# Kernel tuning notes

Measured on AMD Instinct MI355X. Metric: run time of the kernel, lower is better.

The kernel has to match this reference:

```python
import jax, jax.numpy as jnp
import numpy as np

HIDDEN = 1024
HEADS = 16
HEAD_DIM = HIDDEN // HEADS


def setup_inputs() -> dict:
    key = jax.random.key(0)
    ks = jax.random.split(key, 4)
    B, S, H = 2, 2048, HIDDEN
    scale = 1.0 / np.sqrt(H)
    return {
        "inputs": jax.random.normal(ks[0], (B, S, H), dtype=jnp.float32),
        "mask": jnp.ones((B, S), dtype=jnp.int32),
        "Wq": jax.random.normal(ks[1], (H, H), dtype=jnp.float32) * scale,
        "bq": jnp.zeros((H,), dtype=jnp.float32),
        "Wk": jax.random.normal(ks[2], (H, H), dtype=jnp.float32) * scale,
        "bk": jnp.zeros((H,), dtype=jnp.float32),
        "Wv": jax.random.normal(ks[3], (H, H), dtype=jnp.float32) * scale,
        "bv": jnp.zeros((H,), dtype=jnp.float32),
    }


def _split_heads(x, B, S):
    # [B,S,H] -> [B,heads,S,head_dim]
    return x.reshape(B, S, HEADS, HEAD_DIM).transpose(0, 2, 1, 3)


def reference(inputs, mask, Wq, bq, Wk, bk, Wv, bv):
    B, S, H = inputs.shape
    q = _split_heads(inputs @ Wq.T + bq, B, S)
    k = _split_heads(inputs @ Wk.T + bk, B, S)
    v = _split_heads(inputs @ Wv.T + bv, B, S)
    scores = jnp.einsum("bhqd,bhkd->bhqk", q, k) / jnp.sqrt(
        jnp.asarray(HEAD_DIM, dtype=inputs.dtype))
    # mask broadcast [B,1,1,S]; zeros -> -inf
    scores = jnp.where(mask[:, None, None, :] == 0, -jnp.inf, scores)
    attn = jax.nn.softmax(scores, axis=-1)
    context = jnp.einsum("bhqk,bhkd->bhqd", attn, v)
    return context.transpose(0, 2, 1, 3).reshape(B, S, H)
```

## Files before the change

kernel.cpp:

```cpp
#include <hip/hip_runtime.h>
#include <hip/hip_fp16.h>

constexpr int S_LEN  = 2048;
constexpr int HID    = 1024;
constexpr int HEADS  = 16;
constexpr int HDIM   = 64;
constexpr int BATCH  = 2;
constexpr int BH     = BATCH * HEADS;
constexpr int M_ROWS = BATCH * S_LEN;

typedef _Float16 half8  __attribute__((ext_vector_type(8)));
typedef _Float16 half4v __attribute__((ext_vector_type(4)));
typedef _Float16 half2v __attribute__((ext_vector_type(2)));
typedef float    f32x4  __attribute__((ext_vector_type(4)));
typedef float    f32x16 __attribute__((ext_vector_type(16)));
typedef unsigned uint4v __attribute__((ext_vector_type(4)));

constexpr float EXP2_OFF = -11.541560327111707f;
constexpr float Q_SCALE  = 0.18033688011112042f;

__global__ __launch_bounds__(256) void cvt_kernel(
    const float* __restrict__ X,  const float* __restrict__ Wq,
    const float* __restrict__ Wk, const float* __restrict__ Wv,
    const int* __restrict__ mask,
    _Float16* __restrict__ Xh,  _Float16* __restrict__ Wqh,
    _Float16* __restrict__ Wkh, _Float16* __restrict__ Wvh,
    float* __restrict__ maskF)
{
    const int blk = blockIdx.x;
    if (blk >= 3584) {
        const int loc = blk - 3584;
        const size_t e = ((size_t)loc * 256 + threadIdx.x) * 8;
        #pragma unroll
        for (int i = 0; i < 8; ++i)
            maskF[e + i] = mask[e + i] ? EXP2_OFF : -1.0e30f;
        return;
    }
    const float* src; _Float16* dst; int loc;
    if (blk < 2048)      { src = X;  dst = Xh;  loc = blk; }
    else if (blk < 2560) { src = Wq; dst = Wqh; loc = blk - 2048; }
    else if (blk < 3072) { src = Wk; dst = Wkh; loc = blk - 2560; }
    else                 { src = Wv; dst = Wvh; loc = blk - 3072; }
    const size_t e = ((size_t)loc * 256 + threadIdx.x) * 8;
    float4 a = *reinterpret_cast<const float4*>(&src[e]);
    float4 b = *reinterpret_cast<const float4*>(&src[e + 4]);
    half8 h = { (_Float16)a.x, (_Float16)a.y, (_Float16)a.z, (_Float16)a.w,
                (_Float16)b.x, (_Float16)b.y, (_Float16)b.z, (_Float16)b.w };
    *reinterpret_cast<half8*>(&dst[e]) = h;
}

__device__ __forceinline__ void async_cp16(_Float16* lds, const _Float16* g) {
    __builtin_amdgcn_global_load_lds(
        (const __attribute__((address_space(1))) void*)g,
        (__attribute__((address_space(3))) void*)lds, 16, 0, 0);
}
__device__ __forceinline__ void async_cp4(float* lds, const float* g) {
    __builtin_amdgcn_global_load_lds(
        (const __attribute__((address_space(1))) void*)g,
        (__attribute__((address_space(3))) void*)lds, 4, 0, 0);
}

__device__ __forceinline__ void permlane32_swap(unsigned &x, unsigned &y) {
    asm("v_permlane32_swap_b32 %0, %1" : "+v"(x), "+v"(y));
}

__global__ __launch_bounds__(256) void qkv_proj_kernel(
    const _Float16* __restrict__ Xh,
    const _Float16* __restrict__ Wqh, const _Float16* __restrict__ Wkh,
    const _Float16* __restrict__ Wvh,
    const float* __restrict__ bq, const float* __restrict__ bk,
    const float* __restrict__ bv,
    _Float16* __restrict__ Qo, _Float16* __restrict__ Ko,
    _Float16* __restrict__ Vt)
{
    const int mode = blockIdx.z;
    const _Float16* W    = (mode == 0) ? Wqh : (mode == 1) ? Wkh : Wvh;
    const float*    bias = (mode == 0) ? bq  : (mode == 1) ? bk  : bv;

    const int m0 = blockIdx.x * 128, n0 = blockIdx.y * 128;
    const int tid = threadIdx.x, wave = tid >> 6, lane = tid & 63;
    const int l31 = lane & 31, kg = lane >> 5;

    __shared__ _Float16 SMEM[18432];

    f32x16 acc[2][2];
    #pragma unroll
    for (int mt = 0; mt < 2; ++mt)
        #pragma unroll
        for (int nt = 0; nt < 2; ++nt)
            #pragma unroll
            for (int i = 0; i < 16; ++i) acc[mt][nt][i] = 0.f;

    const int wm = (wave & 1) * 64, wn = (wave >> 1) * 64;

    const int srow = tid >> 2, spos = tid & 3;
    auto stage = [&](int k0, int b) {
        _Float16* Asb = SMEM + b * 8192;
        _Float16* Bsb = Asb + 4096;
        #pragma unroll
        for (int j = 0; j < 2; ++j) {
            const int row = srow + j * 64;
            const int sch = spos ^ (row & 3);
            async_cp16(&Asb[j * 2048 + tid * 8],
                       &Xh[(size_t)(m0 + row) * HID + k0 + sch * 8]);
            async_cp16(&Bsb[j * 2048 + tid * 8],
                       &W [(size_t)(n0 + row) * HID + k0 + sch * 8]);
        }
    };

    stage(0, 0);
    int buf = 0;

    for (int k0 = 0; k0 < HID; k0 += 32) {
        __syncthreads();
        if (k0 + 32 < HID) stage(k0 + 32, buf ^ 1);
        _Float16* Asb = SMEM + buf * 8192;
        _Float16* Bsb = Asb + 4096;

        #pragma unroll
        for (int c = 0; c < 2; ++c) {
            const int k8 = c * 2 + kg;
            half8 af[2], bf[2];
            #pragma unroll
            for (int mt = 0; mt < 2; ++mt) {
                const int row = wm + mt * 32 + l31;
                af[mt] = *reinterpret_cast<const half8*>(
                    &Asb[row * 32 + ((k8 ^ (row & 3)) * 8)]);
            }
            #pragma unroll
            for (int nt = 0; nt < 2; ++nt) {
                const int row = wn + nt * 32 + l31;
                bf[nt] = *reinterpret_cast<const half8*>(
                    &Bsb[row * 32 + ((k8 ^ (row & 3)) * 8)]);
            }
            #pragma unroll
            for (int mt = 0; mt < 2; ++mt)
                #pragma unroll
                for (int nt = 0; nt < 2; ++nt)
                    acc[mt][nt] = __builtin_amdgcn_mfma_f32_32x32x16_f16(
                        af[mt], bf[nt], acc[mt][nt], 0, 0, 0);
        }
        buf ^= 1;
    }
    __syncthreads();

    _Float16* T = SMEM + wave * 4608;

    const int nn  = n0 + wn;
    const int hh  = nn >> 6;
    const int mm  = m0 + wm;
    const int bb  = mm >> 11;
    const int bhv = bb * HEADS + hh;
    const int s0  = mm & 2047;
    const int rowg = lane >> 3, chunk = lane & 7;

    if (mode < 2) {
        _Float16* Out = (mode == 0) ? Qo : Ko;
        #pragma unroll
        for (int nt = 0; nt < 2; ++nt) {
            const int col = nt * 32 + l31;
            float bias_n = bias[nn + col];
            #pragma unroll
            for (int mt = 0; mt < 2; ++mt)
                #pragma unroll
                for (int r = 0; r < 16; ++r) {
                    const int row_l = (r & 3) + 8 * (r >> 2) + 4 * kg;
                    float v = acc[mt][nt][r] + bias_n;
                    if (mode == 0) v *= Q_SCALE;
                    T[(mt * 32 + row_l) * 72 + col] = (_Float16)v;
                }
        }
        asm volatile("s_waitcnt lgkmcnt(0)" ::: "memory");
        #pragma unroll
        for (int j = 0; j < 8; ++j) {
            const int sr = j * 8 + rowg;
            half8 v = *reinterpret_cast<const half8*>(&T[sr * 72 + chunk * 8]);
            *reinterpret_cast<half8*>(
                &Out[((size_t)bhv * S_LEN + s0 + sr) * HDIM + chunk * 8]) = v;
        }
    } else {
        #pragma unroll
        for (int nt = 0; nt < 2; ++nt) {
            const int col = nt * 32 + l31;
            const float bias_n = bias[nn + col];
            #pragma unroll
            for (int mt = 0; mt < 2; ++mt)
                #pragma unroll
                for (int rg = 0; rg < 4; ++rg) {
                    half4v t = { (_Float16)(acc[mt][nt][rg * 4 + 0] + bias_n),
                                 (_Float16)(acc[mt][nt][rg * 4 + 1] + bias_n),
                                 (_Float16)(acc[mt][nt][rg * 4 + 2] + bias_n),
                                 (_Float16)(acc[mt][nt][rg * 4 + 3] + bias_n) };
                    const int s_off = mt * 32 + 8 * rg + 4 * kg;
                    *reinterpret_cast<half4v*>(&T[col * 72 + s_off]) = t;
                }
        }
        asm volatile("s_waitcnt lgkmcnt(0)" ::: "memory");
        #pragma unroll
        for (int j = 0; j < 8; ++j) {
            const int dr = j * 8 + rowg;
            half8 v = *reinterpret_cast<const half8*>(&T[dr * 72 + chunk * 8]);
            *reinterpret_cast<half8*>(
                &Vt[((size_t)bhv * HDIM + dr) * S_LEN + s0 + chunk * 8]) = v;
        }
    }
}

__global__ __launch_bounds__(256) void attn_kernel(
    const _Float16* __restrict__ Q, const _Float16* __restrict__ K,
    const _Float16* __restrict__ Vt, const float* __restrict__ maskF,
    float* __restrict__ Out)
{
    const int id   = blockIdx.x;
    const int xcd  = id & 7;
    const int bh   = xcd * 4 + ((id >> 3) & 3);
    const int qt   = id >> 5;
    const int b = bh >> 4, h = bh & 15;
    const int tid = threadIdx.x, wave = tid >> 6, lane = tid & 63;
    const int l31 = lane & 31, kg = lane >> 5;

    __shared__ _Float16 Ks[3][64 * 64];
    __shared__ _Float16 Vs[3][64 * 64];
    __shared__ float    Ms[3][4][64];

    const _Float16* Qb = Q  + (size_t)bh * S_LEN * HDIM;
    const _Float16* Kb = K  + (size_t)bh * S_LEN * HDIM;
    const _Float16* Vb = Vt + (size_t)bh * HDIM * S_LEN;
    const float*    mb = maskF + b * S_LEN;

    const int qrow = qt * 128 + wave * 32 + l31;

    half8 qf[4];
    #pragma unroll
    for (int kc = 0; kc < 4; ++kc)
        qf[kc] = *reinterpret_cast<const half8*>(
            &Qb[(size_t)qrow * HDIM + kc * 16 + kg * 8]);
    asm volatile("s_waitcnt vmcnt(0)" ::: "memory");

    f32x16 acc[2];
    #pragma unroll
    for (int dt = 0; dt < 2; ++dt)
        #pragma unroll
        for (int i = 0; i < 16; ++i) acc[dt][i] = 0.f;
    float den = 0.f;

    const int srow_t = tid >> 3;
    const int slot   = tid & 7;
    auto stage = [&](int tile, int bufsel) {
        const int kb = tile * 64;
        #pragma unroll
        for (int j = 0; j < 2; ++j) {
            const int row  = srow_t + j * 32;
            const int csrc = slot ^ (row & 7);
            async_cp16(&Ks[bufsel][j * 2048 + tid * 8],
                       &Kb[(size_t)(kb + row) * HDIM + csrc * 8]);
            async_cp16(&Vs[bufsel][j * 2048 + tid * 8],
                       &Vb[(size_t)row * S_LEN + kb + csrc * 8]);
        }
        async_cp4(&Ms[bufsel][wave][lane], &mb[kb + lane]);
    };

    constexpr int NT = S_LEN / 64;
    stage(0, 0);
    stage(1, 1);
    int buf = 0;
    const int rsw = l31 & 7;

    for (int t = 0; t < NT; ++t) {
        asm volatile("s_waitcnt vmcnt(5)" ::: "memory");
        __builtin_amdgcn_s_barrier();
        asm volatile("" ::: "memory");

        {
            int nt2 = t + 2; if (nt2 >= NT) nt2 -= NT;
            int nb  = buf + 2; if (nb >= 3) nb -= 3;
            stage(nt2, nb);
        }

        const _Float16* Kl = Ks[buf];
        const _Float16* Vl = Vs[buf];
        const float*    Mw = Ms[buf][wave];

        f32x16 sc[2];
        #pragma unroll
        for (int kt = 0; kt < 2; ++kt) {
            #pragma unroll
            for (int i = 0; i < 16; ++i) sc[kt][i] = 0.f;
            half8 kf[4];
            #pragma unroll
            for (int kc = 0; kc < 4; ++kc)
                kf[kc] = *reinterpret_cast<const half8*>(
                    &Kl[(kt * 32 + l31) * 64 + (((kc * 2 + kg) ^ rsw) * 8)]);
            __builtin_amdgcn_s_setprio(1);
            #pragma unroll
            for (int kc = 0; kc < 4; ++kc)
                sc[kt] = __builtin_amdgcn_mfma_f32_32x32x16_f16(
                    kf[kc], qf[kc], sc[kt], 0, 0, 0);
            __builtin_amdgcn_s_setprio(0);
        }

        half8 vf[2][4];
        #pragma unroll
        for (int dt = 0; dt < 2; ++dt)
            #pragma unroll
            for (int kc = 0; kc < 4; ++kc)
                vf[dt][kc] = *reinterpret_cast<const half8*>(
                    &Vl[(dt * 32 + l31) * 64 + (((kc * 2 + kg) ^ rsw) * 8)]);

        #pragma unroll
        for (int kt = 0; kt < 2; ++kt) {
            float4 mm[4];
            #pragma unroll
            for (int g = 0; g < 4; ++g)
                mm[g] = *reinterpret_cast<const float4*>(
                    &Mw[kt * 32 + g * 8 + kg * 4]);

            float p[16];
            #pragma unroll
            for (int r = 0; r < 16; ++r) {
                const float* m4 = reinterpret_cast<const float*>(&mm[r >> 2]);
                p[r] = __builtin_amdgcn_exp2f(sc[kt][r] + m4[r & 3]);
            }
            den += (((p[0] + p[1]) + (p[2] + p[3])) +
                    ((p[4] + p[5]) + (p[6] + p[7]))) +
                   (((p[8] + p[9]) + (p[10] + p[11])) +
                    ((p[12] + p[13]) + (p[14] + p[15])));

            #pragma unroll
            for (int hh = 0; hh < 2; ++hh) {
                unsigned a0 = __builtin_bit_cast(unsigned,
                    __builtin_amdgcn_cvt_pkrtz(p[hh * 8 + 0], p[hh * 8 + 1]));
                unsigned a1 = __builtin_bit_cast(unsigned,
                    __builtin_amdgcn_cvt_pkrtz(p[hh * 8 + 2], p[hh * 8 + 3]));
                unsigned b0 = __builtin_bit_cast(unsigned,
                    __builtin_amdgcn_cvt_pkrtz(p[hh * 8 + 4], p[hh * 8 + 5]));
                unsigned b1 = __builtin_bit_cast(unsigned,
                    __builtin_amdgcn_cvt_pkrtz(p[hh * 8 + 6], p[hh * 8 + 7]));
                permlane32_swap(a0, b0);
                permlane32_swap(a1, b1);
                uint4v pd = { a0, a1, b0, b1 };
                half8 pf = __builtin_bit_cast(half8, pd);
                const int kc2 = kt * 2 + hh;
                __builtin_amdgcn_s_setprio(1);
                acc[0] = __builtin_amdgcn_mfma_f32_32x32x16_f16(
                    vf[0][kc2], pf, acc[0], 0, 0, 0);
                acc[1] = __builtin_amdgcn_mfma_f32_32x32x16_f16(
                    vf[1][kc2], pf, acc[1], 0, 0, 0);
                __builtin_amdgcn_s_setprio(0);
            }
        }
        if (++buf == 3) buf = 0;
    }

    den += __shfl_xor(den, 32, 64);
    const float inv = 1.0f / den;

    float* orow = Out + ((size_t)(b * S_LEN + qrow)) * HID + h * HDIM;
    #pragma unroll
    for (int dt = 0; dt < 2; ++dt)
        #pragma unroll
        for (int g = 0; g < 4; ++g) {
            float4 o = { acc[dt][g * 4 + 0] * inv, acc[dt][g * 4 + 1] * inv,
                         acc[dt][g * 4 + 2] * inv, acc[dt][g * 4 + 3] * inv };
            *reinterpret_cast<float4*>(&orow[dt * 32 + g * 8 + kg * 4]) = o;
        }
}

extern "C" void kernel_launch(void* const* d_in, const int* in_sizes, int n_in,
                              void* d_out, int out_size, void* d_ws, size_t ws_size,
                              hipStream_t stream) {
    const float* X  = (const float*)d_in[0];
    const int*   mk = (const int*)  d_in[1];
    const float* Wq = (const float*)d_in[2];
    const float* bq = (const float*)d_in[3];
    const float* Wk = (const float*)d_in[4];
    const float* bk = (const float*)d_in[5];
    const float* Wv = (const float*)d_in[6];
    const float* bv = (const float*)d_in[7];
    float* out = (float*)d_out;

    _Float16* Xh  = (_Float16*)d_ws;
    _Float16* Wqh = Xh  + (size_t)M_ROWS * HID;
    _Float16* Wkh = Wqh + (size_t)HID * HID;
    _Float16* Wvh = Wkh + (size_t)HID * HID;
    _Float16* Q   = Wvh + (size_t)HID * HID;
    _Float16* K   = Q   + (size_t)BH * S_LEN * HDIM;
    _Float16* Vt  = K   + (size_t)BH * S_LEN * HDIM;
    float*    maskF = (float*)(Vt + (size_t)BH * S_LEN * HDIM);

    cvt_kernel<<<3586, 256, 0, stream>>>(X, Wq, Wk, Wv, mk, Xh, Wqh, Wkh, Wvh, maskF);

    dim3 gp(M_ROWS / 128, HID / 128, 3);
    qkv_proj_kernel<<<gp, 256, 0, stream>>>(Xh, Wqh, Wkh, Wvh, bq, bk, bv, Q, K, Vt);

    attn_kernel<<<512, 256, 0, stream>>>(Q, K, Vt, maskF, out);
}
```

Measured before the change: 179.2 us.

## Split attention key tiles across two wave groups with LDS reduction

Attention blocks grow from 4 to 8 waves. Each pair of waves shares a 32-row query strip and takes one half of every 64-key tile, so each wave does half the QK and PV MFMA work per tile. Partial accumulators and denominators are summed through shared memory at the end. The mask is now preloaded into the score accumulator instead of added before exp, saving per-element adds. This adds more waves per CU to hide latency, at the cost of extra barriers, an LDS reduction and higher register-limited occupancy pressure.

```diff
diff --git a/kernel.cpp b/kernel.cpp
--- a/kernel.cpp
+++ b/kernel.cpp
@@ -206,7 +206,7 @@
     }
 }
 
-__global__ __launch_bounds__(256) void attn_kernel(
+__global__ __launch_bounds__(512, 4) void attn_kernel(
     const _Float16* __restrict__ Q, const _Float16* __restrict__ K,
     const _Float16* __restrict__ Vt, const float* __restrict__ maskF,
     float* __restrict__ Out)
@@ -218,17 +218,17 @@
     const int b = bh >> 4, h = bh & 15;
     const int tid = threadIdx.x, wave = tid >> 6, lane = tid & 63;
     const int l31 = lane & 31, kg = lane >> 5;
-
-    __shared__ _Float16 Ks[3][64 * 64];
-    __shared__ _Float16 Vs[3][64 * 64];
-    __shared__ float    Ms[3][4][64];
+    const int wq = wave & 3, wk = wave >> 2;
+
+    __shared__ _Float16 SMEM[3 * 8192];
+    __shared__ float    Ms[3][8][64];
 
     const _Float16* Qb = Q  + (size_t)bh * S_LEN * HDIM;
     const _Float16* Kb = K  + (size_t)bh * S_LEN * HDIM;
     const _Float16* Vb = Vt + (size_t)bh * HDIM * S_LEN;
     const float*    mb = maskF + b * S_LEN;
 
-    const int qrow = qt * 128 + wave * 32 + l31;
+    const int qrow = qt * 128 + wq * 32 + l31;
 
     half8 qf[4];
     #pragma unroll
@@ -244,19 +244,15 @@
         for (int i = 0; i < 16; ++i) acc[dt][i] = 0.f;
     float den = 0.f;
 
-    const int srow_t = tid >> 3;
-    const int slot   = tid & 7;
+    const int srow = tid >> 3;
+    const int slot = tid & 7;
     auto stage = [&](int tile, int bufsel) {
-        const int kb = tile * 64;
-        #pragma unroll
-        for (int j = 0; j < 2; ++j) {
-            const int row  = srow_t + j * 32;
-            const int csrc = slot ^ (row & 7);
-            async_cp16(&Ks[bufsel][j * 2048 + tid * 8],
-                       &Kb[(size_t)(kb + row) * HDIM + csrc * 8]);
-            async_cp16(&Vs[bufsel][j * 2048 + tid * 8],
-                       &Vb[(size_t)row * S_LEN + kb + csrc * 8]);
-        }
+        const int kb   = tile * 64;
+        const int csrc = slot ^ (srow & 7);
+        _Float16* Kd = SMEM + bufsel * 8192;
+        _Float16* Vd = Kd + 4096;
+        async_cp16(&Kd[tid * 8], &Kb[(size_t)(kb + srow) * HDIM + csrc * 8]);
+        async_cp16(&Vd[tid * 8], &Vb[(size_t)srow * S_LEN + kb + csrc * 8]);
         async_cp4(&Ms[bufsel][wave][lane], &mb[kb + lane]);
     };
 
@@ -267,7 +263,7 @@
     const int rsw = l31 & 7;
 
     for (int t = 0; t < NT; ++t) {
-        asm volatile("s_waitcnt vmcnt(5)" ::: "memory");
+        asm volatile("s_waitcnt vmcnt(3)" ::: "memory");
         __builtin_amdgcn_s_barrier();
         asm volatile("" ::: "memory");
 
@@ -277,93 +273,111 @@
             stage(nt2, nb);
         }
 
-        const _Float16* Kl = Ks[buf];
-        const _Float16* Vl = Vs[buf];
+        const _Float16* Kl = SMEM + buf * 8192;
+        const _Float16* Vl = Kl + 4096;
         const float*    Mw = Ms[buf][wave];
 
-        f32x16 sc[2];
-        #pragma unroll
-        for (int kt = 0; kt < 2; ++kt) {
-            #pragma unroll
-            for (int i = 0; i < 16; ++i) sc[kt][i] = 0.f;
-            half8 kf[4];
-            #pragma unroll
-            for (int kc = 0; kc < 4; ++kc)
-                kf[kc] = *reinterpret_cast<const half8*>(
-                    &Kl[(kt * 32 + l31) * 64 + (((kc * 2 + kg) ^ rsw) * 8)]);
+        float4 mm0 = *reinterpret_cast<const float4*>(&Mw[wk * 32 + 0 + kg * 4]);
+        float4 mm1 = *reinterpret_cast<const float4*>(&Mw[wk * 32 + 8 + kg * 4]);
+        float4 mm2 = *reinterpret_cast<const float4*>(&Mw[wk * 32 + 16 + kg * 4]);
+        float4 mm3 = *reinterpret_cast<const float4*>(&Mw[wk * 32 + 24 + kg * 4]);
+        f32x16 sc = { mm0.x, mm0.y, mm0.z, mm0.w,
+                      mm1.x, mm1.y, mm1.z, mm1.w,
+                      mm2.x, mm2.y, mm2.z, mm2.w,
+                      mm3.x, mm3.y, mm3.z, mm3.w };
+
+        const _Float16* Krow = &Kl[(wk * 32 + l31) * 64];
+        half8 kf[4];
+        #pragma unroll
+        for (int kc = 0; kc < 4; ++kc)
+            kf[kc] = *reinterpret_cast<const half8*>(
+                &Krow[((kc * 2 + kg) ^ rsw) * 8]);
+        __builtin_amdgcn_s_setprio(1);
+        #pragma unroll
+        for (int kc = 0; kc < 4; ++kc)
+            sc = __builtin_amdgcn_mfma_f32_32x32x16_f16(kf[kc], qf[kc], sc, 0, 0, 0);
+        __builtin_amdgcn_s_setprio(0);
+
+        half8 vf[2][2];
+        #pragma unroll
+        for (int dt = 0; dt < 2; ++dt) {
+            const _Float16* Vrow = &Vl[(dt * 32 + l31) * 64];
+            #pragma unroll
+            for (int hh = 0; hh < 2; ++hh)
+                vf[dt][hh] = *reinterpret_cast<const half8*>(
+                    &Vrow[((wk * 4 + hh * 2 + kg) ^ rsw) * 8]);
+        }
+
+        float p[16];
+        #pragma unroll
+        for (int r = 0; r < 16; ++r)
+            p[r] = __builtin_amdgcn_exp2f(sc[r]);
+        den += (((p[0] + p[1]) + (p[2] + p[3])) +
+                ((p[4] + p[5]) + (p[6] + p[7]))) +
+               (((p[8] + p[9]) + (p[10] + p[11])) +
+                ((p[12] + p[13]) + (p[14] + p[15])));
+
+        #pragma unroll
+        for (int hh = 0; hh < 2; ++hh) {
+            unsigned a0 = __builtin_bit_cast(unsigned,
+                __builtin_amdgcn_cvt_pkrtz(p[hh * 8 + 0], p[hh * 8 + 1]));
+            unsigned a1 = __builtin_bit_cast(unsigned,
+                __builtin_amdgcn_cvt_pkrtz(p[hh * 8 + 2], p[hh * 8 + 3]));
+            unsigned b0 = __builtin_bit_cast(unsigned,
+                __builtin_amdgcn_cvt_pkrtz(p[hh * 8 + 4], p[hh * 8 + 5]));
+            unsigned b1 = __builtin_bit_cast(unsigned,
+                __builtin_amdgcn_cvt_pkrtz(p[hh * 8 + 6], p[hh * 8 + 7]));
+            permlane32_swap(a0, b0);
+            permlane32_swap(a1, b1);
+            uint4v pd = { a0, a1, b0, b1 };
+            half8 pf = __builtin_bit_cast(half8, pd);
             __builtin_amdgcn_s_setprio(1);
-            #pragma unroll
-            for (int kc = 0; kc < 4; ++kc)
-                sc[kt] = __builtin_amdgcn_mfma_f32_32x32x16_f16(
-                    kf[kc], qf[kc], sc[kt], 0, 0, 0);
+            acc[0] = __builtin_amdgcn_mfma_f32_32x32x16_f16(
+                vf[0][hh], pf, acc[0], 0, 0, 0);
+            acc[1] = __builtin_amdgcn_mfma_f32_32x32x16_f16(
+                vf[1][hh], pf, acc[1], 0, 0, 0);
             __builtin_amdgcn_s_setprio(0);
         }
-
-        half8 vf[2][4];
+        if (++buf == 3) buf = 0;
+    }
+
+    asm volatile("s_waitcnt vmcnt(0)" ::: "memory");
+    __syncthreads();
+
+    den += __shfl_xor(den, 32, 64);
+
+    float* LF = reinterpret_cast<float*>(SMEM);
+    float* DF = reinterpret_cast<float*>(Ms);
+    if (wk == 1) {
+        float* wbase = LF + (wq * 64 + lane) * 36;
         #pragma unroll
         for (int dt = 0; dt < 2; ++dt)
             #pragma unroll
-            for (int kc = 0; kc < 4; ++kc)
-                vf[dt][kc] = *reinterpret_cast<const half8*>(
-                    &Vl[(dt * 32 + l31) * 64 + (((kc * 2 + kg) ^ rsw) * 8)]);
-
-        #pragma unroll
-        for (int kt = 0; kt < 2; ++kt) {
-            float4 mm[4];
-            #pragma unroll
-            for (int g = 0; g < 4; ++g)
-                mm[g] = *reinterpret_cast<const float4*>(
-                    &Mw[kt * 32 + g * 8 + kg * 4]);
-
-            float p[16];
-            #pragma unroll
-            for (int r = 0; r < 16; ++r) {
-                const float* m4 = reinterpret_cast<const float*>(&mm[r >> 2]);
-                p[r] = __builtin_amdgcn_exp2f(sc[kt][r] + m4[r & 3]);
+            for (int g = 0; g < 4; ++g) {
+                float4 o = { acc[dt][g * 4 + 0], acc[dt][g * 4 + 1],
+                             acc[dt][g * 4 + 2], acc[dt][g * 4 + 3] };
+                *reinterpret_cast<float4*>(&wbase[dt * 16 + g * 4]) = o;
             }
-            den += (((p[0] + p[1]) + (p[2] + p[3])) +
-                    ((p[4] + p[5]) + (p[6] + p[7]))) +
-                   (((p[8] + p[9]) + (p[10] + p[11])) +
-                    ((p[12] + p[13]) + (p[14] + p[15])));
-
-            #pragma unroll
-            for (int hh = 0; hh < 2; ++hh) {
-                unsigned a0 = __builtin_bit_cast(unsigned,
-                    __builtin_amdgcn_cvt_pkrtz(p[hh * 8 + 0], p[hh * 8 + 1]));
-                unsigned a1 = __builtin_bit_cast(unsigned,
-                    __builtin_amdgcn_cvt_pkrtz(p[hh * 8 + 2], p[hh * 8 + 3]));
-                unsigned b0 = __builtin_bit_cast(unsigned,
-                    __builtin_amdgcn_cvt_pkrtz(p[hh * 8 + 4], p[hh * 8 + 5]));
-                unsigned b1 = __builtin_bit_cast(unsigned,
-                    __builtin_amdgcn_cvt_pkrtz(p[hh * 8 + 6], p[hh * 8 + 7]));
-                permlane32_swap(a0, b0);
-                permlane32_swap(a1, b1);
-                uint4v pd = { a0, a1, b0, b1 };
-                half8 pf = __builtin_bit_cast(half8, pd);
-                const int kc2 = kt * 2 + hh;
-                __builtin_amdgcn_s_setprio(1);
-                acc[0] = __builtin_amdgcn_mfma_f32_32x32x16_f16(
-                    vf[0][kc2], pf, acc[0], 0, 0, 0);
-                acc[1] = __builtin_amdgcn_mfma_f32_32x32x16_f16(
-                    vf[1][kc2], pf, acc[1], 0, 0, 0);
-                __builtin_amdgcn_s_setprio(0);
+        if (kg == 0) DF[wq * 32 + l31] = den;
+    }
+    __syncthreads();
+    if (wk == 0) {
+        const float* rbase = LF + (wq * 64 + lane) * 36;
+        const float inv = 1.0f / (den + DF[wq * 32 + l31]);
+        float* orow = Out + ((size_t)(b * S_LEN + qrow)) * HID + h * HDIM;
+        #pragma unroll
+        for (int dt = 0; dt < 2; ++dt)
+            #pragma unroll
+            for (int g = 0; g < 4; ++g) {
+                float4 pv = *reinterpret_cast<const float4*>(
+                    &rbase[dt * 16 + g * 4]);
+                float4 o = { (acc[dt][g * 4 + 0] + pv.x) * inv,
+                             (acc[dt][g * 4 + 1] + pv.y) * inv,
+                             (acc[dt][g * 4 + 2] + pv.z) * inv,
+                             (acc[dt][g * 4 + 3] + pv.w) * inv };
+                *reinterpret_cast<float4*>(&orow[dt * 32 + g * 8 + kg * 4]) = o;
             }
-        }
-        if (++buf == 3) buf = 0;
-    }
-
-    den += __shfl_xor(den, 32, 64);
-    const float inv = 1.0f / den;
-
-    float* orow = Out + ((size_t)(b * S_LEN + qrow)) * HID + h * HDIM;
-    #pragma unroll
-    for (int dt = 0; dt < 2; ++dt)
-        #pragma unroll
-        for (int g = 0; g < 4; ++g) {
-            float4 o = { acc[dt][g * 4 + 0] * inv, acc[dt][g * 4 + 1] * inv,
-                         acc[dt][g * 4 + 2] * inv, acc[dt][g * 4 + 3] * inv };
-            *reinterpret_cast<float4*>(&orow[dt * 32 + g * 8 + kg * 4]) = o;
-        }
+    }
 }
 
 extern "C" void kernel_launch(void* const* d_in, const int* in_sizes, int n_in,
@@ -393,5 +407,5 @@
     dim3 gp(M_ROWS / 128, HID / 128, 3);
     qkv_proj_kernel<<<gp, 256, 0, stream>>>(Xh, Wqh, Wkh, Wvh, bq, bk, bv, Q, K, Vt);
 
-    attn_kernel<<<512, 256, 0, stream>>>(Q, K, Vt, maskF, out);
-}
+    attn_kernel<<<512, 512, 0, stream>>>(Q, K, Vt, maskF, out);
+}
```

After: 169.0 us. 1.06x faster.
